# Kernel optimization log

Measured on AMD Instinct MI355X. Metric: run time of the kernel, lower is better.

The kernel has to match this reference:

```python
import jax, jax.numpy as jnp
import numpy as np

INDIM, OUTDIM, K, EXPAND = 256, 256, 3, 64
STRIDE, PAD, DIL, GROUPS = 1, 1, 1, 1


def _make_mask(rng):
    # expander connectivity: indim == outdim, so use the 'else' branch of the
    # torch code: for each input channel, pick EXPAND output channels.
    m = np.zeros((OUTDIM, INDIM), dtype=np.float32)
    for i in range(INDIM):
        x = rng.permutation(OUTDIM)[:EXPAND]
        m[x, i] = 1.0
    # repeat over the kernel spatial dims
    return np.broadcast_to(m[:, :, None, None], (OUTDIM, INDIM, K, K)).copy()


def setup_inputs() -> dict:
    key = jax.random.key(0)
    k1, k2 = jax.random.split(key)
    x = jax.random.normal(k1, (32, INDIM, 56, 56), dtype=jnp.float32)
    # kaiming_normal_(mode='fan_out'): std = sqrt(2 / (outdim * k * k))
    std = np.sqrt(2.0 / (OUTDIM * K * K)).astype(np.float32)
    weight = jax.random.normal(k2, (OUTDIM, INDIM, K, K), dtype=jnp.float32) * std
    mask = jnp.asarray(_make_mask(np.random.default_rng(0)))
    return {"x": x, "weight": weight, "mask": mask}


def reference(x, weight, mask) -> jnp.ndarray:
    w = weight * mask  # zero out non-expander connections
    return jax.lax.conv_general_dilated(
        x, w,
        window_strides=(STRIDE, STRIDE),
        padding=((PAD, PAD), (PAD, PAD)),
        rhs_dilation=(DIL, DIL),
        feature_group_count=GROUPS,
        dimension_numbers=("NCHW", "OIHW", "NCHW"),
    )
```

## Files before the change

kernel.cpp:

```cpp
#include <hip/hip_runtime.h>
#include <hip/hip_bf16.h>

typedef short short8 __attribute__((ext_vector_type(8)));
typedef float float4v __attribute__((ext_vector_type(4)));

#define NIMG 32
#define CIN 256
#define COUT 256
#define HH 56
#define WW 56
#define HP 58
#define WP 58
#define PIXIMG (HH * WW)
#define TOTPIX (NIMG * PIXIMG)
#define OUTSTRIDE_N (COUT * PIXIMG)

static constexpr size_t XT_ELEMS = (size_t)NIMG * HP * WP * CIN;
static constexpr size_t WT_ELEMS = (size_t)9 * COUT * CIN;

static __device__ __forceinline__ unsigned short f2bf(float f) {
    unsigned int u = __builtin_bit_cast(unsigned int, f);
    u = (u + 0x7fffu + ((u >> 16) & 1u)) >> 16;
    return (unsigned short)u;
}

static __device__ __forceinline__ void gl16(const unsigned short* g, char* l) {
    __builtin_amdgcn_global_load_lds(
        (const __attribute__((address_space(1))) void*)g,
        (__attribute__((address_space(3))) void*)l, 16, 0, 0);
}

__global__ __launch_bounds__(256) void k_transpose(const float* __restrict__ x,
                                                   unsigned short* __restrict__ xt) {
    int b   = blockIdx.x;
    int icb = b & 3;
    int hp  = (b >> 2) % HP;
    int n   = b / (4 * HP);
    unsigned short* rowb = xt + ((size_t)(n * HP + hp) * WP) * CIN + icb * 64;
    int t = threadIdx.x;

    if (hp == 0 || hp == HP - 1) {
        for (int idx = t; idx < WP * 8; idx += 256) {
            int wq = idx >> 3, q = idx & 7;
            *(uint4*)(rowb + (size_t)wq * CIN + q * 8) = (uint4){0, 0, 0, 0};
        }
        return;
    }
    int h = hp - 1;
    __shared__ __align__(16) char lds[64 * 128];
    int w = t & 63, icl0 = t >> 6;
    if (w < WW) {
        const float* src = x + ((size_t)(n * CIN + icb * 64 + icl0) * HH + h) * WW + w;
#pragma unroll
        for (int j = 0; j < 16; ++j) {
            float v = src[(size_t)(j * 4) * PIXIMG];
            int icl = icl0 + j * 4;
            *(unsigned short*)(lds + w * 128 + ((icl * 2) ^ ((w & 7) << 4))) = f2bf(v);
        }
    }
    __syncthreads();
    int ic4 = t & 15, wr = t >> 4;
    unsigned short* dst = rowb + (size_t)CIN + ic4 * 4;
#pragma unroll
    for (int p = 0; p < 4; ++p) {
        int w2 = wr + p * 16;
        if (w2 < WW) {
            uint2 v = *(const uint2*)(lds + w2 * 128 + ((ic4 * 8) ^ ((w2 & 7) << 4)));
            *(uint2*)(dst + (size_t)w2 * CIN) = v;
        }
    }
    if (t < 32) {
        int col = (t >> 4) * (WP - 1);
        *(uint2*)(rowb + (size_t)col * CIN + (t & 15) * 4) = (uint2){0, 0};
    }
}

__global__ __launch_bounds__(256) void k_prepw(const float* __restrict__ wgt,
                                               const float* __restrict__ msk,
                                               unsigned short* __restrict__ wt) {
    int t = blockIdx.x * 256 + threadIdx.x;
    const float* wp = wgt + (size_t)t * 9;
    const float* mp = msk + (size_t)t * 9;
#pragma unroll
    for (int tap = 0; tap < 9; ++tap)
        wt[(size_t)tap * (COUT * CIN) + t] = f2bf(wp[tap] * mp[tap]);
}

__global__ __launch_bounds__(256, 4) void k_conv(const unsigned short* __restrict__ xt,
                                                 const unsigned short* __restrict__ wt,
                                                 float* __restrict__ out) {
    __shared__ __align__(16) char lds[64 * 132 * 4];

    const int t    = threadIdx.x;
    const int lane = t & 63;
    const int wid  = t >> 6;
    const int woc  = wid >> 1;
    const int wpx  = wid & 1;

    const int b0 = blockIdx.x;
    const int b  = (b0 & 7) * 196 + (b0 >> 3);
    const int ptile = b >> 1;
    const int ocb   = b & 1;

    const int rl  = lane >> 3;
    const int sc  = ((lane & 7) ^ rl) * 8;
    const unsigned short* aS[4];
    const unsigned short* bS[4];
    char* dA[4];
    char* dB[4];
#pragma unroll
    for (int c = 0; c < 4; ++c) {
        int r = wid * 32 + c * 8 + rl;
        aS[c] = wt + (size_t)(ocb * 128 + r) * CIN + sc;
        int pg  = ptile * 128 + r;
        int n   = pg / PIXIMG;
        int rem = pg - n * PIXIMG;
        int h   = rem / WW, w = rem - h * WW;
        bS[c] = xt + ((size_t)((n * HP + h) * WP + w)) * CIN + sc;
        dA[c] = lds + (wid * 32 + c * 8) * 128;
        dB[c] = lds + 16384 + (wid * 32 + c * 8) * 128;
    }

    const int l15  = lane & 15;
    const int lg   = lane >> 4;
    const int swzf = (lane & 7) << 4;
    int colk[2];
    colk[0] = (lg * 16) ^ swzf;
    colk[1] = (64 + lg * 16) ^ swzf;
    int rowA[4], rowB[4];
#pragma unroll
    for (int i = 0; i < 4; ++i) {
        rowA[i] = (woc * 64 + i * 16 + l15) * 128;
        rowB[i] = 16384 + (wpx * 64 + i * 16 + l15) * 128;
    }

    float4v acc[4][4];
#pragma unroll
    for (int i = 0; i < 4; ++i)
#pragma unroll
        for (int j = 0; j < 4; ++j)
            acc[i][j] = (float4v){0.f, 0.f, 0.f, 0.f};

#pragma unroll 1
    for (int s = 0; s < 36; ++s) {
        const int tap = s >> 2;
        const int dh  = (tap * 86) >> 8;
        const int dw  = tap - dh * 3;
        const size_t ao = (size_t)tap * (COUT * CIN) + (size_t)((s & 3) << 6);
        const size_t bo = (size_t)(dh * WP + dw) * CIN + (size_t)((s & 3) << 6);
#pragma unroll
        for (int c = 0; c < 4; ++c) gl16(aS[c] + ao, dA[c]);
#pragma unroll
        for (int c = 0; c < 4; ++c) gl16(bS[c] + bo, dB[c]);
        __syncthreads();
#pragma unroll
        for (int kk = 0; kk < 2; ++kk) {
            short8 af[4], bfr[4];
#pragma unroll
            for (int i = 0; i < 4; ++i)
                af[i] = *(const short8*)(lds + rowA[i] + colk[kk]);
#pragma unroll
            for (int i = 0; i < 4; ++i)
                bfr[i] = *(const short8*)(lds + rowB[i] + colk[kk]);
#pragma unroll
            for (int oi = 0; oi < 4; ++oi)
#pragma unroll
                for (int pi = 0; pi < 4; ++pi)
                    acc[oi][pi] = __builtin_amdgcn_mfma_f32_16x16x32_bf16(
                        af[oi], bfr[pi], acc[oi][pi], 0, 0, 0);
        }
        __syncthreads();
    }

    float* ep = (float*)lds;
#pragma unroll 1
    for (int c = 0; c < 2; ++c) {
        if (woc == c) {
#pragma unroll
            for (int oi = 0; oi < 4; ++oi)
#pragma unroll
                for (int pi = 0; pi < 4; ++pi)
#pragma unroll
                    for (int r = 0; r < 4; ++r)
                        ep[(oi * 16 + lg * 4 + r) * 132 +
                           (wpx * 64 + pi * 16 + l15)] = acc[oi][pi][r];
        }
        __syncthreads();
        const int rrow = t >> 5;
        const int rcol = (t & 31) * 4;
        int pg  = ptile * 128 + rcol;
        int n2  = pg / PIXIMG;
        int rem = pg - n2 * PIXIMG;
        float* ob = out + (size_t)n2 * OUTSTRIDE_N +
                    (size_t)(ocb * 128 + c * 64) * PIXIMG + rem;
#pragma unroll
        for (int rd = 0; rd < 8; ++rd) {
            int row = rd * 8 + rrow;
            float4v v = *(const float4v*)&ep[row * 132 + rcol];
            *(float4v*)(ob + (size_t)row * PIXIMG) = v;
        }
        __syncthreads();
    }
}

__global__ __launch_bounds__(256) void k_naive(const float* __restrict__ x,
                                               const float* __restrict__ wg,
                                               const float* __restrict__ mk,
                                               float* __restrict__ out, int total) {
    int idx = blockIdx.x * 256 + threadIdx.x;
    if (idx >= total) return;
    int w  = idx % WW;
    int h  = (idx / WW) % HH;
    int oc = (idx / PIXIMG) % COUT;
    int n  = idx / (COUT * PIXIMG);
    float s = 0.f;
    for (int ic = 0; ic < CIN; ++ic) {
        const float* xp = x + (size_t)(n * CIN + ic) * PIXIMG;
        const float* wp = wg + (size_t)(oc * CIN + ic) * 9;
        const float* mp = mk + (size_t)(oc * CIN + ic) * 9;
#pragma unroll
        for (int kh = 0; kh < 3; ++kh) {
            int hy = h + kh - 1;
            if ((unsigned)hy >= HH) continue;
#pragma unroll
            for (int kw = 0; kw < 3; ++kw) {
                int wx = w + kw - 1;
                if ((unsigned)wx >= WW) continue;
                s += xp[hy * WW + wx] * wp[kh * 3 + kw] * mp[kh * 3 + kw];
            }
        }
    }
    out[idx] = s;
}

extern "C" void kernel_launch(void* const* d_in, const int* in_sizes, int n_in,
                              void* d_out, int out_size, void* d_ws, size_t ws_size,
                              hipStream_t stream) {
    const float* x  = (const float*)d_in[0];
    const float* wg = (const float*)d_in[1];
    const float* mk = (const float*)d_in[2];
    float* out = (float*)d_out;

    size_t need = XT_ELEMS * 2 + WT_ELEMS * 2 + 256;
    if (ws_size < need) {
        int total = NIMG * COUT * PIXIMG;
        k_naive<<<(total + 255) / 256, 256, 0, stream>>>(x, wg, mk, out, total);
        return;
    }

    unsigned short* xt = (unsigned short*)d_ws;
    unsigned short* wt = (unsigned short*)((char*)d_ws + XT_ELEMS * 2);

    k_transpose<<<NIMG * HP * 4, 256, 0, stream>>>(x, xt);
    k_prepw<<<(COUT * CIN) / 256, 256, 0, stream>>>(wg, mk, wt);
    k_conv<<<(TOTPIX / 128) * 2, 256, 0, stream>>>(xt, wt, out);
}
```

Baseline: 152.2 us.

## Double-buffer LDS with K=32 stages and reduce shared memory footprint

The main loop is restructured from 36 single-buffered K=64 stages into 72 K=32 stages across two LDS buffers, so global-to-LDS loads for the next stage are issued before computing on the current one, with explicit vmcnt waits and barriers. The LDS layout moves to 64-byte rows with a new XOR swizzle, and the epilogue is split into four quarter tiles so total LDS stays at 32KB. This aims to hide global load latency behind MFMA work, at the cost of more barriers per unit of K and more epilogue passes.

```diff
diff --git a/kernel.cpp b/kernel.cpp
--- a/kernel.cpp
+++ b/kernel.cpp
@@ -89,7 +89,7 @@
 __global__ __launch_bounds__(256, 4) void k_conv(const unsigned short* __restrict__ xt,
                                                  const unsigned short* __restrict__ wt,
                                                  float* __restrict__ out) {
-    __shared__ __align__(16) char lds[64 * 132 * 4];
+    __shared__ __align__(16) char lds[32768];
 
     const int t    = threadIdx.x;
     const int lane = t & 63;
@@ -102,36 +102,34 @@
     const int ptile = b >> 1;
     const int ocb   = b & 1;
 
-    const int rl  = lane >> 3;
-    const int sc  = ((lane & 7) ^ rl) * 8;
-    const unsigned short* aS[4];
-    const unsigned short* bS[4];
-    char* dA[4];
-    char* dB[4];
-#pragma unroll
-    for (int c = 0; c < 4; ++c) {
-        int r = wid * 32 + c * 8 + rl;
+    const int rl = lane >> 2;
+    const int sc = ((lane & 3) ^ (rl & 3)) * 8;
+    const unsigned short* aS[2];
+    const unsigned short* bS[2];
+    char* dA[2];
+    char* dB[2];
+#pragma unroll
+    for (int c = 0; c < 2; ++c) {
+        int r = wid * 32 + c * 16 + rl;
         aS[c] = wt + (size_t)(ocb * 128 + r) * CIN + sc;
         int pg  = ptile * 128 + r;
         int n   = pg / PIXIMG;
         int rem = pg - n * PIXIMG;
         int h   = rem / WW, w = rem - h * WW;
         bS[c] = xt + ((size_t)((n * HP + h) * WP + w)) * CIN + sc;
-        dA[c] = lds + (wid * 32 + c * 8) * 128;
-        dB[c] = lds + 16384 + (wid * 32 + c * 8) * 128;
-    }
-
-    const int l15  = lane & 15;
-    const int lg   = lane >> 4;
-    const int swzf = (lane & 7) << 4;
-    int colk[2];
-    colk[0] = (lg * 16) ^ swzf;
-    colk[1] = (64 + lg * 16) ^ swzf;
+        dA[c] = lds + (wid * 32 + c * 16) * 64;
+        dB[c] = lds + 8192 + (wid * 32 + c * 16) * 64;
+    }
+
+    const int l15 = lane & 15;
+    const int lg  = lane >> 4;
     int rowA[4], rowB[4];
 #pragma unroll
     for (int i = 0; i < 4; ++i) {
-        rowA[i] = (woc * 64 + i * 16 + l15) * 128;
-        rowB[i] = 16384 + (wpx * 64 + i * 16 + l15) * 128;
+        int ra = woc * 64 + i * 16 + l15;
+        int rb = wpx * 64 + i * 16 + l15;
+        rowA[i] = ra * 64 + ((lg * 16) ^ ((ra & 3) << 4));
+        rowB[i] = 8192 + rb * 64 + ((lg * 16) ^ ((rb & 3) << 4));
     }
 
     float4v acc[4][4];
@@ -141,62 +139,92 @@
         for (int j = 0; j < 4; ++j)
             acc[i][j] = (float4v){0.f, 0.f, 0.f, 0.f};
 
+#define STAGE(BUF, S)                                                        \
+    do {                                                                     \
+        const int tap_ = (S) >> 3, icq_ = (S) & 7;                           \
+        const int dh_ = (tap_ * 86) >> 8, dw_ = tap_ - dh_ * 3;              \
+        const size_t ao_ = (size_t)tap_ * (COUT * CIN) + icq_ * 32;          \
+        const size_t bo_ = (size_t)(dh_ * WP + dw_) * CIN + icq_ * 32;       \
+        gl16(aS[0] + ao_, dA[0] + (BUF));                                    \
+        gl16(aS[1] + ao_, dA[1] + (BUF));                                    \
+        gl16(bS[0] + bo_, dB[0] + (BUF));                                    \
+        gl16(bS[1] + bo_, dB[1] + (BUF));                                    \
+    } while (0)
+
+#define COMP(BUF)                                                            \
+    do {                                                                     \
+        short8 af_[4], bf_[4];                                               \
+        _Pragma("unroll")                                                    \
+        for (int i_ = 0; i_ < 4; ++i_)                                       \
+            af_[i_] = *(const short8*)(lds + (BUF) + rowA[i_]);              \
+        _Pragma("unroll")                                                    \
+        for (int i_ = 0; i_ < 4; ++i_)                                       \
+            bf_[i_] = *(const short8*)(lds + (BUF) + rowB[i_]);              \
+        _Pragma("unroll")                                                    \
+        for (int oi_ = 0; oi_ < 4; ++oi_)                                    \
+            _Pragma("unroll")                                                \
+            for (int pi_ = 0; pi_ < 4; ++pi_)                                \
+                acc[oi_][pi_] = __builtin_amdgcn_mfma_f32_16x16x32_bf16(     \
+                    af_[oi_], bf_[pi_], acc[oi_][pi_], 0, 0, 0);             \
+    } while (0)
+
+#define BAR do { asm volatile("s_waitcnt lgkmcnt(0)" ::: "memory");          \
+                 __builtin_amdgcn_s_barrier();                               \
+                 asm volatile("" ::: "memory"); } while (0)
+#define VMW4 asm volatile("s_waitcnt vmcnt(4)" ::: "memory")
+#define VMW0 asm volatile("s_waitcnt vmcnt(0)" ::: "memory")
+
+    STAGE(0, 0);
+
 #pragma unroll 1
-    for (int s = 0; s < 36; ++s) {
-        const int tap = s >> 2;
-        const int dh  = (tap * 86) >> 8;
-        const int dw  = tap - dh * 3;
-        const size_t ao = (size_t)tap * (COUT * CIN) + (size_t)((s & 3) << 6);
-        const size_t bo = (size_t)(dh * WP + dw) * CIN + (size_t)((s & 3) << 6);
-#pragma unroll
-        for (int c = 0; c < 4; ++c) gl16(aS[c] + ao, dA[c]);
-#pragma unroll
-        for (int c = 0; c < 4; ++c) gl16(bS[c] + bo, dB[c]);
-        __syncthreads();
-#pragma unroll
-        for (int kk = 0; kk < 2; ++kk) {
-            short8 af[4], bfr[4];
-#pragma unroll
-            for (int i = 0; i < 4; ++i)
-                af[i] = *(const short8*)(lds + rowA[i] + colk[kk]);
-#pragma unroll
-            for (int i = 0; i < 4; ++i)
-                bfr[i] = *(const short8*)(lds + rowB[i] + colk[kk]);
-#pragma unroll
-            for (int oi = 0; oi < 4; ++oi)
-#pragma unroll
-                for (int pi = 0; pi < 4; ++pi)
-                    acc[oi][pi] = __builtin_amdgcn_mfma_f32_16x16x32_bf16(
-                        af[oi], bfr[pi], acc[oi][pi], 0, 0, 0);
-        }
-        __syncthreads();
-    }
+    for (int it = 0; it < 35; ++it) {
+        const int s1 = 2 * it + 1;
+        STAGE(16384, s1);
+        VMW4; BAR;
+        COMP(0);
+        BAR;
+        STAGE(0, s1 + 1);
+        VMW4; BAR;
+        COMP(16384);
+        BAR;
+    }
+    STAGE(16384, 71);
+    VMW4; BAR;
+    COMP(0);
+    BAR;
+    VMW0; BAR;
+    COMP(16384);
+    BAR;
+#undef STAGE
+#undef COMP
 
     float* ep = (float*)lds;
 #pragma unroll 1
-    for (int c = 0; c < 2; ++c) {
-        if (woc == c) {
+    for (int q = 0; q < 4; ++q) {
+        const int c = q >> 1;
+        const int p = q & 1;
+        if (woc == c && wpx == p) {
 #pragma unroll
             for (int oi = 0; oi < 4; ++oi)
 #pragma unroll
                 for (int pi = 0; pi < 4; ++pi)
 #pragma unroll
                     for (int r = 0; r < 4; ++r)
-                        ep[(oi * 16 + lg * 4 + r) * 132 +
-                           (wpx * 64 + pi * 16 + l15)] = acc[oi][pi][r];
+                        ep[(oi * 16 + lg * 4 + r) * 68 + (pi * 16 + l15)] =
+                            acc[oi][pi][r];
         }
         __syncthreads();
-        const int rrow = t >> 5;
-        const int rcol = (t & 31) * 4;
-        int pg  = ptile * 128 + rcol;
+        const int erow0 = t >> 4;
+        const int ecol  = (t & 15) * 4;
+        int pg  = ptile * 128 + p * 64 + ecol;
         int n2  = pg / PIXIMG;
         int rem = pg - n2 * PIXIMG;
         float* ob = out + (size_t)n2 * OUTSTRIDE_N +
                     (size_t)(ocb * 128 + c * 64) * PIXIMG + rem;
 #pragma unroll
-        for (int rd = 0; rd < 8; ++rd) {
-            int row = rd * 8 + rrow;
-            float4v v = *(const float4v*)&ep[row * 132 + rcol];
+        for (int rd = 0; rd < 4; ++rd) {
+            int row = rd * 16 + erow0;
+            float4v v = *(const float4v*)&ep[row * 68 + ecol];
             *(float4v*)(ob + (size_t)row * PIXIMG) = v;
         }
         __syncthreads();
```

Measured after the change: 178.9 us. 1.18x slower.
